# Kernel tuning notes

Hardware: AMD Instinct MI355X
Metric: run time of the kernel (lower is better)

Reference implementation:

```python
import jax, jax.numpy as jnp
import numpy as np
from jax import lax

# ---- module hyperparams (from __init__ defaults) ----
REF_TR = 2.0
NUM_BANDS = 5
FREQ_LO, FREQ_HI = 0.008, 0.12

# ---- pywt.cwt('morl') internals, precision=10 ----
NPSI = 1024                                   # 2**10 samples of the wavelet
_x = np.linspace(-8.0, 8.0, NPSI)             # morlet support [-8, 8]
STEP = float(_x[1] - _x[0])
DOMAIN = 16.0                                 # x[-1] - x[0]
_psi = np.exp(-_x ** 2 / 2.0) * np.cos(5.0 * _x)   # 'morl' wavelet psi(t)
INT_PSI = jnp.asarray(np.cumsum(_psi) * STEP, dtype=jnp.float32)  # integrate_wavelet
LMAX = 544                                    # static bound: max scale ~33.4 -> L <= 535


def _cwt_band(gpad, scale):
    """pywt conv-method CWT at one scale for all regions.
    gpad: [R, N+1+2*LMAX] = first difference of zero-extended signal, zero-padded.
    Uses identity: diff(convolve(x, K[::-1])) == correlate(diff-ext(x), K) shifted.
    """
    R = gpad.shape[0]
    N = gpad.shape[1] - 1 - 2 * LMAX
    i = jnp.arange(LMAX)
    # len(np.arange(scale*16 + 1)) for non-integer scale*16
    L0 = jnp.floor(scale * DOMAIN).astype(jnp.int32) + 2
    j = jnp.floor(i.astype(jnp.float32) / (scale * STEP)).astype(jnp.int32)
    mask = (i < L0) & (j < NPSI)              # pywt filters j < int_psi.size
    K = jnp.where(mask, INT_PSI[jnp.clip(j, 0, NPSI - 1)], 0.0)  # int_psi_scale (unreversed)
    L = mask.sum()                            # effective kernel length (mask is a prefix)
    # cross-correlation of gpad with K (lax.conv does correlation, no kernel flip)
    corr = lax.conv_general_dilated(gpad[:, None, :], K[None, None, :], (1,), 'VALID',
                                    dimension_numbers=('NCH', 'OIH', 'NCH'))[:, 0, :]
    # center crop: coef[t] = -sqrt(s) * (c[t+f+1]-c[t+f]),  f = floor((L-2)/2)
    start = LMAX + (L - 2) // 2 + 2 - L
    coef = lax.dynamic_slice(corr, (jnp.int32(0), start), (R, N))
    return jnp.abs(-jnp.sqrt(scale) * coef)


def _forward(timeseries, tr_values, log_scale_params, bandwidth_params):
    B, R, N = timeseries.shape
    tr_factors = tr_values / REF_TR
    scales = jnp.exp(log_scale_params)[None, :] / tr_factors[:, None]      # [B, bands]
    # frequency bands [B, bands, 2]
    center = 1.0 / (scales * tr_values[:, None])
    bw = bandwidth_params[None, :]
    low = jnp.maximum(FREQ_LO, center * (1.0 - bw / 2.0))
    high = jnp.minimum(FREQ_HI, center * (1.0 + bw / 2.0))
    frequency_bands = jnp.stack([low, high], axis=-1)
    # first difference of zero-extended signal: g[m] = x[m] - x[m-1], x=0 outside [0,N)
    g = jnp.diff(jnp.pad(timeseries, ((0, 0), (0, 0), (1, 1))), axis=-1)    # [B,R,N+1]
    gpad = jnp.pad(g, ((0, 0), (0, 0), (LMAX, LMAX)))
    per_sample = jax.vmap(_cwt_band, in_axes=(None, 0))                     # over bands
    coeffs = jax.vmap(per_sample, in_axes=(0, 0))(gpad, scales)             # [B,bands,R,N]
    coeffs = jnp.transpose(coeffs, (0, 2, 1, 3))                            # [B,R,bands,N]
    return coeffs, frequency_bands


def setup_inputs() -> dict:
    key = jax.random.key(0)
    k1, k2 = jax.random.split(key)
    B, R, T = 8, 400, 1200
    timeseries = jax.random.normal(k1, (B, R, T), dtype=jnp.float32)
    # realistic fMRI TRs in [1.5, 2.5] s (keeps adaptive scales <= 33.4 < LMAX/16)
    tr_values = 1.5 + jax.random.uniform(k2, (B,), dtype=jnp.float32)
    log_scale_params = jnp.linspace(np.log(5.0), np.log(25.0), NUM_BANDS).astype(jnp.float32)
    bandwidth_params = 0.1 * jnp.ones((NUM_BANDS,), dtype=jnp.float32)
    return {"timeseries": timeseries, "tr_values": tr_values,
            "log_scale_params": log_scale_params, "bandwidth_params": bandwidth_params}


def reference(timeseries, tr_values, log_scale_params, bandwidth_params):
    return _forward(timeseries, tr_values, log_scale_params, bandwidth_params)
```

## Files before the change

kernel.cpp:

```cpp
#include <hip/hip_runtime.h>
#include <math.h>

#define B_    8
#define R_    400
#define N_    1200
#define S_    5
#define LMAX_ 544
#define NPSI_ 1024
#define KPAD  560
#define WINMAX 1792
#define T_    19
#define C_    24
#define WSZ   24

#define WS_K      0
#define WS_SCALE  (40*KPAD)
#define WS_SQS    (WS_SCALE + 40)
#define WS_LPAD   (WS_SQS + 40)
#define WS_WST    (WS_LPAD + 40)

__global__ __launch_bounds__(256) void setup_kernel(
    const float* __restrict__ tr,
    const float* __restrict__ lsp,
    const float* __restrict__ bwp,
    float* __restrict__ ws,
    float* __restrict__ out_bands)
{
    __shared__ double psi_sh[NPSI_];
    __shared__ float  intpsi[NPSI_];
    __shared__ double wtot[4];
    __shared__ float  scale_sh[40];
    __shared__ int    cnt_sh[40];
    const double STEP_D = 16.0 / 1023.0;
    const float  STEP_F = (float)(16.0 / 1023.0);
    const int tid = threadIdx.x;

    if (tid < 40) cnt_sh[tid] = 0;

    for (int k = tid; k < NPSI_; k += 256) {
        double x = (k == NPSI_ - 1) ? 8.0 : (-8.0 + (double)k * STEP_D);
        psi_sh[k] = exp(-x * x * 0.5) * cos(5.0 * x);
    }
    __syncthreads();

    {
        double a0 = psi_sh[4 * tid + 0], a1 = psi_sh[4 * tid + 1];
        double a2 = psi_sh[4 * tid + 2], a3 = psi_sh[4 * tid + 3];
        double s1 = a0 + a1, s2 = s1 + a2, s3 = s2 + a3;
        double run = s3;
        #pragma unroll
        for (int d = 1; d < 64; d <<= 1) {
            double o = __shfl_up(run, (unsigned)d, 64);
            if ((tid & 63) >= d) run += o;
        }
        if ((tid & 63) == 63) wtot[tid >> 6] = run;
        __syncthreads();
        double woff = 0.0;
        const int w = tid >> 6;
        #pragma unroll
        for (int k = 0; k < 4; ++k) if (k < w) woff += wtot[k];
        double excl = woff + run - s3;
        intpsi[4 * tid + 0] = (float)((excl + a0) * STEP_D);
        intpsi[4 * tid + 1] = (float)((excl + s1) * STEP_D);
        intpsi[4 * tid + 2] = (float)((excl + s2) * STEP_D);
        intpsi[4 * tid + 3] = (float)((excl + s3) * STEP_D);
    }

    if (tid < 40) {
        int b = tid / S_, s = tid % S_;
        float trf   = tr[b] / 2.0f;
        float scale = expf(lsp[s]) / trf;
        scale_sh[tid] = scale;
        ws[WS_SQS + tid] = sqrtf(scale);
        float center = 1.0f / (scale * tr[b]);
        float bw = bwp[s];
        out_bands[2 * tid + 0] = fmaxf(0.008f, center * (1.0f - bw * 0.5f));
        out_bands[2 * tid + 1] = fminf(0.12f,  center * (1.0f + bw * 0.5f));
    }
    __syncthreads();

    {
        const int wv = tid >> 6, ln = tid & 63;
        for (int c = wv; c < 40 * 9; c += 4) {
            int p = c / 9, i = (c % 9) * 64 + ln;
            float scale = scale_sh[p];
            float sst   = scale * STEP_F;
            int   L0    = (int)floorf(scale * 16.0f) + 2;
            bool m = false;
            if (i < LMAX_) {
                int j = (int)floorf((float)i / sst);
                m = (i < L0) && (j < NPSI_);
            }
            unsigned long long bal = __ballot(m);
            if (ln == 0) atomicAdd(&cnt_sh[p], __popcll(bal));
        }
    }
    __syncthreads();
    if (tid < 40) {
        int L = cnt_sh[tid];
        ((int*)(ws + WS_LPAD))[tid] = ((L + C_ - 1) / C_) * C_;
        ((int*)(ws + WS_WST))[tid]  = (L - 2) / 2 + 2 - L;
    }

    for (int idx = tid; idx < 40 * KPAD; idx += 256) {
        int p = idx / KPAD, i = idx % KPAD;
        float v = 0.0f;
        if (i < LMAX_) {
            float scale = scale_sh[p];
            float sst   = scale * STEP_F;
            int   L0    = (int)floorf(scale * 16.0f) + 2;
            int   j     = (int)floorf((float)i / sst);
            if (i < L0 && j < NPSI_) {
                int jc = j < 0 ? 0 : (j > NPSI_ - 1 ? NPSI_ - 1 : j);
                v = intpsi[jc];
            }
        }
        ws[WS_K + idx] = v;
    }
}

__global__ __launch_bounds__(128) void cwt_main_kernel(
    const float* __restrict__ ts,
    const float* __restrict__ ws,
    float* __restrict__ out)
{
    const float* __restrict__ Kbase = ws + WS_K;
    const float* sqs_arr  = ws + WS_SQS;
    const int*   Lpad_arr = (const int*)(ws + WS_LPAD);
    const int*   wst_arr  = (const int*)(ws + WS_WST);

    const int bid = blockIdx.x;
    const int s   = 4 - bid / 1600;
    const int rem = bid % 1600;
    const int b   = rem / 200;
    const int rp  = rem % 200;
    const int pair = b * S_ + s;

    const int   Lpad   = Lpad_arr[pair];
    const int   wstart = wst_arr[pair];
    const float sqs    = sqs_arr[pair];

    __shared__ float gwin[2][WINMAX];
    const int tid = threadIdx.x;

    for (int rr = 0; rr < 2; ++rr) {
        const float* tsrow = ts + (size_t)(b * R_ + rp * 2 + rr) * N_;
        for (int t = tid; t < WINMAX; t += 128) {
            int k = wstart + t;
            float v = 0.0f;
            if (k >= 0 && k <= N_) {
                float a = (k < N_) ? tsrow[k]     : 0.0f;
                float c = (k > 0)  ? tsrow[k - 1] : 0.0f;
                v = a - c;
            }
            gwin[rr][t] = v;
        }
    }
    __syncthreads();

    const int wv = tid >> 6;
    const int ln = tid & 63;
    const int t0 = T_ * ln;
    const float* gw = &gwin[wv][0];
    const float* __restrict__ Kp = Kbase + pair * KPAD;

    float acc[T_];
    #pragma unroll
    for (int q = 0; q < T_; ++q) acc[q] = 0.0f;

    float W[WSZ];
    #pragma unroll
    for (int x = 0; x < WSZ; ++x) W[x] = gw[t0 + x];

    for (int i = 0; i < Lpad; i += C_) {
        #pragma unroll
        for (int u = 0; u < C_; ++u) {
            const float kv = Kp[i + u];
            #pragma unroll
            for (int q = 0; q < T_; ++q)
                acc[q] = fmaf(kv, W[(u + q) % WSZ], acc[q]);
            W[u] = gw[t0 + i + u + WSZ];
        }
    }

    {
        const int r = rp * 2 + wv;
        float* op = out + ((size_t)(b * R_ + r) * S_ + s) * N_;
        #pragma unroll
        for (int q = 0; q < T_; ++q) {
            int t = t0 + q;
            if (t < N_) op[t] = sqs * fabsf(acc[q]);
        }
    }
}

extern "C" void kernel_launch(void* const* d_in, const int* in_sizes, int n_in,
                              void* d_out, int out_size, void* d_ws, size_t ws_size,
                              hipStream_t stream)
{
    const float* ts  = (const float*)d_in[0];
    const float* tr  = (const float*)d_in[1];
    const float* lsp = (const float*)d_in[2];
    const float* bwp = (const float*)d_in[3];
    float* out = (float*)d_out;
    float* ws  = (float*)d_ws;
    float* out_bands = out + (size_t)B_ * R_ * S_ * N_;

    hipLaunchKernelGGL(setup_kernel, dim3(1), dim3(256), 0, stream,
                       tr, lsp, bwp, ws, out_bands);
    hipLaunchKernelGGL(cwt_main_kernel, dim3(8000), dim3(128), 0, stream,
                       ts, ws, out);
}
```

Before: 225.1 us.

## Stage kernel taps in LDS with double-buffered registers and parallelize setup

```diff
diff --git a/kernel.cpp b/kernel.cpp
--- a/kernel.cpp
+++ b/kernel.cpp
@@ -7,10 +7,11 @@
 #define S_    5
 #define LMAX_ 544
 #define NPSI_ 1024
-#define KPAD  560
-#define WINMAX 1792
+#define KPAD  576
+#define KLDS  640
+#define WINMAX 1824
 #define T_    19
-#define C_    24
+#define C_    48
 #define WSZ   24
 
 #define WS_K      0
@@ -18,8 +19,9 @@
 #define WS_SQS    (WS_SCALE + 40)
 #define WS_LPAD   (WS_SQS + 40)
 #define WS_WST    (WS_LPAD + 40)
-
-__global__ __launch_bounds__(256) void setup_kernel(
+#define WS_INTPSI (WS_WST + 40)
+
+__global__ __launch_bounds__(256) void setup_a_kernel(
     const float* __restrict__ tr,
     const float* __restrict__ lsp,
     const float* __restrict__ bwp,
@@ -27,15 +29,9 @@
     float* __restrict__ out_bands)
 {
     __shared__ double psi_sh[NPSI_];
-    __shared__ float  intpsi[NPSI_];
     __shared__ double wtot[4];
-    __shared__ float  scale_sh[40];
-    __shared__ int    cnt_sh[40];
     const double STEP_D = 16.0 / 1023.0;
-    const float  STEP_F = (float)(16.0 / 1023.0);
     const int tid = threadIdx.x;
-
-    if (tid < 40) cnt_sh[tid] = 0;
 
     for (int k = tid; k < NPSI_; k += 256) {
         double x = (k == NPSI_ - 1) ? 8.0 : (-8.0 + (double)k * STEP_D);
@@ -60,62 +56,68 @@
         #pragma unroll
         for (int k = 0; k < 4; ++k) if (k < w) woff += wtot[k];
         double excl = woff + run - s3;
-        intpsi[4 * tid + 0] = (float)((excl + a0) * STEP_D);
-        intpsi[4 * tid + 1] = (float)((excl + s1) * STEP_D);
-        intpsi[4 * tid + 2] = (float)((excl + s2) * STEP_D);
-        intpsi[4 * tid + 3] = (float)((excl + s3) * STEP_D);
+        ws[WS_INTPSI + 4 * tid + 0] = (float)((excl + a0) * STEP_D);
+        ws[WS_INTPSI + 4 * tid + 1] = (float)((excl + s1) * STEP_D);
+        ws[WS_INTPSI + 4 * tid + 2] = (float)((excl + s2) * STEP_D);
+        ws[WS_INTPSI + 4 * tid + 3] = (float)((excl + s3) * STEP_D);
     }
 
     if (tid < 40) {
         int b = tid / S_, s = tid % S_;
         float trf   = tr[b] / 2.0f;
         float scale = expf(lsp[s]) / trf;
-        scale_sh[tid] = scale;
-        ws[WS_SQS + tid] = sqrtf(scale);
+        ws[WS_SCALE + tid] = scale;
+        ws[WS_SQS + tid]   = sqrtf(scale);
         float center = 1.0f / (scale * tr[b]);
         float bw = bwp[s];
         out_bands[2 * tid + 0] = fmaxf(0.008f, center * (1.0f - bw * 0.5f));
         out_bands[2 * tid + 1] = fminf(0.12f,  center * (1.0f + bw * 0.5f));
     }
-    __syncthreads();
-
-    {
-        const int wv = tid >> 6, ln = tid & 63;
-        for (int c = wv; c < 40 * 9; c += 4) {
-            int p = c / 9, i = (c % 9) * 64 + ln;
-            float scale = scale_sh[p];
-            float sst   = scale * STEP_F;
-            int   L0    = (int)floorf(scale * 16.0f) + 2;
-            bool m = false;
-            if (i < LMAX_) {
-                int j = (int)floorf((float)i / sst);
-                m = (i < L0) && (j < NPSI_);
-            }
-            unsigned long long bal = __ballot(m);
-            if (ln == 0) atomicAdd(&cnt_sh[p], __popcll(bal));
-        }
-    }
-    __syncthreads();
-    if (tid < 40) {
-        int L = cnt_sh[tid];
-        ((int*)(ws + WS_LPAD))[tid] = ((L + C_ - 1) / C_) * C_;
-        ((int*)(ws + WS_WST))[tid]  = (L - 2) / 2 + 2 - L;
-    }
-
-    for (int idx = tid; idx < 40 * KPAD; idx += 256) {
-        int p = idx / KPAD, i = idx % KPAD;
+}
+
+__global__ __launch_bounds__(256) void setup_b_kernel(float* __restrict__ ws)
+{
+    const int p   = blockIdx.x;
+    const int tid = threadIdx.x;
+    const float STEP_F = (float)(16.0 / 1023.0);
+
+    const float scale = ws[WS_SCALE + p];
+    const float sst   = scale * STEP_F;
+    const int   L0    = (int)floorf(scale * 16.0f) + 2;
+
+    __shared__ int cnt;
+    if (tid == 0) cnt = 0;
+    __syncthreads();
+
+    const int ln = tid & 63;
+    for (int base = 0; base < LMAX_; base += 256) {
+        int i = base + tid;
+        bool m = false;
+        if (i < LMAX_) {
+            int j = (int)floorf((float)i / sst);
+            m = (i < L0) && (j < NPSI_);
+        }
+        unsigned long long bal = __ballot(m);
+        if (ln == 0) atomicAdd(&cnt, __popcll(bal));
+    }
+
+    for (int i = tid; i < KPAD; i += 256) {
         float v = 0.0f;
         if (i < LMAX_) {
-            float scale = scale_sh[p];
-            float sst   = scale * STEP_F;
-            int   L0    = (int)floorf(scale * 16.0f) + 2;
-            int   j     = (int)floorf((float)i / sst);
+            int j = (int)floorf((float)i / sst);
             if (i < L0 && j < NPSI_) {
                 int jc = j < 0 ? 0 : (j > NPSI_ - 1 ? NPSI_ - 1 : j);
-                v = intpsi[jc];
+                v = ws[WS_INTPSI + jc];
             }
         }
-        ws[WS_K + idx] = v;
+        ws[WS_K + p * KPAD + i] = v;
+    }
+    __syncthreads();
+
+    if (tid == 0) {
+        int L = cnt;
+        ((int*)(ws + WS_LPAD))[p] = ((L + C_ - 1) / C_) * C_;
+        ((int*)(ws + WS_WST))[p]  = (L - 2) / 2 + 2 - L;
     }
 }
 
@@ -141,7 +143,14 @@
     const float sqs    = sqs_arr[pair];
 
     __shared__ float gwin[2][WINMAX];
+    __shared__ __align__(16) float K_lds[KLDS];
     const int tid = threadIdx.x;
+
+    {
+        const float* __restrict__ Kp = Kbase + pair * KPAD;
+        for (int t = tid; t < KLDS; t += 128)
+            K_lds[t] = (t < KPAD) ? Kp[t] : 0.0f;
+    }
 
     for (int rr = 0; rr < 2; ++rr) {
         const float* tsrow = ts + (size_t)(b * R_ + rp * 2 + rr) * N_;
@@ -162,7 +171,6 @@
     const int ln = tid & 63;
     const int t0 = T_ * ln;
     const float* gw = &gwin[wv][0];
-    const float* __restrict__ Kp = Kbase + pair * KPAD;
 
     float acc[T_];
     #pragma unroll
@@ -172,14 +180,31 @@
     #pragma unroll
     for (int x = 0; x < WSZ; ++x) W[x] = gw[t0 + x];
 
+    float kva[24], kvb[24];
+    #pragma unroll
+    for (int m = 0; m < 6; ++m)
+        *(float4*)&kva[4 * m] = *(const float4*)&K_lds[4 * m];
+
     for (int i = 0; i < Lpad; i += C_) {
         #pragma unroll
-        for (int u = 0; u < C_; ++u) {
-            const float kv = Kp[i + u];
+        for (int m = 0; m < 6; ++m)
+            *(float4*)&kvb[4 * m] = *(const float4*)&K_lds[i + 24 + 4 * m];
+        #pragma unroll
+        for (int u = 0; u < 24; ++u) {
             #pragma unroll
             for (int q = 0; q < T_; ++q)
-                acc[q] = fmaf(kv, W[(u + q) % WSZ], acc[q]);
+                acc[q] = fmaf(kva[u], W[(u + q) % WSZ], acc[q]);
             W[u] = gw[t0 + i + u + WSZ];
+        }
+        #pragma unroll
+        for (int m = 0; m < 6; ++m)
+            *(float4*)&kva[4 * m] = *(const float4*)&K_lds[i + 48 + 4 * m];
+        #pragma unroll
+        for (int u = 0; u < 24; ++u) {
+            #pragma unroll
+            for (int q = 0; q < T_; ++q)
+                acc[q] = fmaf(kvb[u], W[(u + q) % WSZ], acc[q]);
+            W[u] = gw[t0 + i + u + 48];
         }
     }
 
@@ -206,8 +231,9 @@
     float* ws  = (float*)d_ws;
     float* out_bands = out + (size_t)B_ * R_ * S_ * N_;
 
-    hipLaunchKernelGGL(setup_kernel, dim3(1), dim3(256), 0, stream,
+    hipLaunchKernelGGL(setup_a_kernel, dim3(1), dim3(256), 0, stream,
                        tr, lsp, bwp, ws, out_bands);
+    hipLaunchKernelGGL(setup_b_kernel, dim3(40), dim3(256), 0, stream, ws);
     hipLaunchKernelGGL(cwt_main_kernel, dim3(8000), dim3(128), 0, stream,
                        ts, ws, out);
 }
```

After: 211.8 us. 5.9% less time.
